# Kernel tuning notes

Hardware: AMD Instinct MI355X
Metric: run time of the kernel (lower is better)

Reference implementation:

```python
import jax, jax.numpy as jnp
import numpy as np

B, N, C, H = 8, 1024, 768, 12
HD = C // H  # 64


def setup_inputs() -> dict:
    key = jax.random.key(0)
    k0, k1, k2, k3, k4 = jax.random.split(key, 5)
    x = jax.random.normal(k0, (B, N, C), jnp.float32)
    # ToMe token sizes are counts >= 1; sample in [1, 16)
    size = jax.random.uniform(k1, (B, N, 1), jnp.float32, minval=1.0, maxval=16.0)
    key_padding_mask = jax.random.randint(k2, (B, N), 0, 2).astype(jnp.bool_)
    w_qkv = jax.random.normal(k3, (3 * C, C), jnp.float32) * (C ** -0.5)
    w_proj = jax.random.normal(k4, (C, C), jnp.float32) * (C ** -0.5)
    b_proj = jnp.zeros((C,), jnp.float32)
    return dict(x=x, size=size, key_padding_mask=key_padding_mask,
                w_qkv=w_qkv, w_proj=w_proj, b_proj=b_proj)


def reference(x, size, key_padding_mask, w_qkv, w_proj, b_proj):
    b, n, c = x.shape
    hd = c // H
    scale = hd ** -0.5
    # qkv projection: [B,N,3C] -> [3,B,H,N,hd]
    qkv = (x @ w_qkv.T).reshape(b, n, 3, H, hd).transpose(2, 0, 3, 1, 4)
    q, k, v = qkv[0], qkv[1], qkv[2]
    # raw scores [B,H,N,N]
    attn = jnp.einsum('bhnd,bhmd->bhnm', q, k) * scale
    # proportional attention: additive log-size bias over keys
    attn = attn + jnp.log(size)[:, None, None, :, 0]
    # key padding mask: True -> -inf
    attn = jnp.where(key_padding_mask[:, None, None, :], -jnp.inf, attn)
    attn = jax.nn.softmax(attn, axis=-1)
    # PV, back to [B,N,C]
    out = jnp.einsum('bhnm,bhmd->bnhd', attn, v).reshape(b, n, c)
    out = out @ w_proj.T + b_proj
    # mean of k over heads: [B,N,hd]
    k_mean = k.mean(axis=1)
    return out, k_mean
```

## Files before the change

### kernel.cpp

```cpp
#include <hip/hip_runtime.h>

typedef __bf16 bf16;
typedef __bf16 bf16x4 __attribute__((ext_vector_type(4)));
typedef __bf16 bf16x8 __attribute__((ext_vector_type(8)));
typedef float f32x4 __attribute__((ext_vector_type(4)));

#define MFMA_16x16x32(a, b, c) __builtin_amdgcn_mfma_f32_16x16x32_bf16((a), (b), (c), 0, 0, 0)

#define B_ 8
#define N_ 1024
#define C_ 768
#define H_ 12
#define HD_ 64
#define KDIM 768

__device__ __forceinline__ void gload_lds16(const void* g, void* l) {
  __builtin_amdgcn_global_load_lds(
      (const __attribute__((address_space(1))) void*)g,
      (__attribute__((address_space(3))) void*)l, 16, 0, 0);
}

__global__ __launch_bounds__(256) void detect_mask_kernel(const unsigned* __restrict__ m32,
                                                          int* __restrict__ flags) {
  const int i = blockIdx.x * 256 + threadIdx.x;
  if (i < 2048) {
    const unsigned v = m32[i];
    if (v > 1u) atomicOr(&flags[0], 1);
    if ((i & 1) && v != 0u) atomicOr(&flags[1], 1);
  }
}

__global__ __launch_bounds__(256) void cvt_kernel(const float* __restrict__ x,
                                                  const float* __restrict__ wq,
                                                  const float* __restrict__ wp,
                                                  const float* __restrict__ size_in,
                                                  const void* __restrict__ mask_raw,
                                                  const int* __restrict__ flags,
                                                  bf16* __restrict__ xb,
                                                  bf16* __restrict__ wqb,
                                                  bf16* __restrict__ wpb,
                                                  float* __restrict__ biasb) {
  const int i = blockIdx.x * 256 + threadIdx.x;
  {
    const float4 v = ((const float4*)x)[i];
    bf16x4 o = {(bf16)v.x, (bf16)v.y, (bf16)v.z, (bf16)v.w};
    ((bf16x4*)xb)[i] = o;
  }
  if (i < 442368) {
    const float4 v = ((const float4*)wq)[i];
    bf16x4 o = {(bf16)v.x, (bf16)v.y, (bf16)v.z, (bf16)v.w};
    ((bf16x4*)wqb)[i] = o;
  }
  if (i < 147456) {
    const float4 v = ((const float4*)wp)[i];
    bf16x4 o = {(bf16)v.x, (bf16)v.y, (bf16)v.z, (bf16)v.w};
    ((bf16x4*)wpb)[i] = o;
  }
  if (i < B_ * N_) {
    int mv;
    if (flags[0]) {
      mv = (int)((const unsigned char*)mask_raw)[i];
    } else if (flags[1]) {
      mv = ((const int*)mask_raw)[i];
    } else {
      const unsigned* m32 = (const unsigned*)mask_raw;
      mv = (int)(m32[2 * i] | m32[2 * i + 1]);
    }
    biasb[i] = mv ? -1e30f : logf(size_in[i]);
  }
}

template <int MODE>
__global__ __launch_bounds__(256) void gemm_bt(const bf16* __restrict__ A,
                                               const bf16* __restrict__ W,
                                               const float* __restrict__ bias,
                                               bf16* __restrict__ out0,
                                               bf16* __restrict__ out1,
                                               bf16* __restrict__ out2,
                                               float* __restrict__ outf) {
  __shared__ bf16 As[128 * 64];
  __shared__ bf16 Bs[128 * 64];
  const int bid = blockIdx.x;
  const int mt = bid % 64;
  const int nt = bid / 64;
  const int t = threadIdx.x;
  const int lane = t & 63, w = t >> 6;
  const int wm = w >> 1, wn = w & 1;
  const int l15 = lane & 15, lg = lane >> 4;

  f32x4 acc[4][4] = {};

  const int srow = t >> 3;
  const int skel = (t & 7) * 8;
  const bf16* Ag = A + (size_t)(mt * 128) * KDIM;
  const bf16* Bg = W + (size_t)(nt * 128) * KDIM;
  const int bA = mt >> 3;
  const int nbase = (mt & 7) * 128;

  for (int kt = 0; kt < KDIM; kt += 64) {
#pragma unroll
    for (int c = 0; c < 4; ++c) {
      const bf16* aSrc;
      if (MODE == 0)
        aSrc = Ag + (size_t)(c * 32 + srow) * KDIM + kt + skel;
      else
        aSrc = A + (((size_t)(bA * 12 + (kt >> 6)) * 1024) + nbase + c * 32 + srow) * 64 + skel;
      gload_lds16(aSrc, (char*)As + c * 4096 + w * 1024);
      gload_lds16(Bg + (size_t)(c * 32 + srow) * KDIM + kt + skel,
                  (char*)Bs + c * 4096 + w * 1024);
    }
    __syncthreads();
#pragma unroll
    for (int ks = 0; ks < 2; ++ks) {
      bf16x8 af[4], bfr[4];
#pragma unroll
      for (int i = 0; i < 4; ++i)
        af[i] = *(const bf16x8*)(As + (wm * 64 + i * 16 + l15) * 64 + ks * 32 + lg * 8);
#pragma unroll
      for (int i = 0; i < 4; ++i)
        bfr[i] = *(const bf16x8*)(Bs + (wn * 64 + i * 16 + l15) * 64 + ks * 32 + lg * 8);
#pragma unroll
      for (int i = 0; i < 4; ++i)
#pragma unroll
        for (int j = 0; j < 4; ++j)
          acc[i][j] = MFMA_16x16x32(af[i], bfr[j], acc[i][j]);
    }
    __syncthreads();
  }

  if (MODE == 0) {
    const int which = (nt * 128) / 768;
#pragma unroll
    for (int i = 0; i < 4; ++i)
#pragma unroll
      for (int j = 0; j < 4; ++j)
#pragma unroll
        for (int r = 0; r < 4; ++r) {
          const int m = mt * 128 + wm * 64 + i * 16 + lg * 4 + r;
          const int o = nt * 128 + wn * 64 + j * 16 + l15;
          const int b = m >> 10, n = m & 1023;
          const int f = o - which * 768;
          const int h = f >> 6, hd = f & 63;
          const bf16 bv = (bf16)acc[i][j][r];
          if (which == 0)
            out0[(((size_t)(b * 12 + h)) * 1024 + n) * 64 + hd] = bv;
          else if (which == 1)
            out1[(((size_t)(b * 12 + h)) * 1024 + n) * 64 + hd] = bv;
          else
            out2[(((size_t)(b * 12 + h)) * 64 + hd) * 1024 + n] = bv;
        }
  } else {
#pragma unroll
    for (int i = 0; i < 4; ++i)
#pragma unroll
      for (int j = 0; j < 4; ++j) {
        const int o = nt * 128 + wn * 64 + j * 16 + l15;
        const float bv = bias[o];
#pragma unroll
        for (int r = 0; r < 4; ++r) {
          const int m = mt * 128 + wm * 64 + i * 16 + lg * 4 + r;
          outf[(size_t)m * 768 + o] = acc[i][j][r] + bv;
        }
      }
  }
}

__global__ __launch_bounds__(256) void kmean_kernel(const bf16* __restrict__ kbuf,
                                                    float* __restrict__ kmean) {
  const int i = blockIdx.x * 256 + threadIdx.x;
  if (i >= B_ * N_ * HD_) return;
  const int hd = i & 63;
  const int n = (i >> 6) & 1023;
  const int b = i >> 16;
  float s = 0.f;
#pragma unroll
  for (int h = 0; h < 12; ++h)
    s += (float)kbuf[(((size_t)(b * 12 + h)) * 1024 + n) * 64 + hd];
  kmean[i] = s * (1.0f / 12.0f);
}

__global__ __launch_bounds__(512, 4) void attn_mfma(const bf16* __restrict__ qbuf,
                                                    const bf16* __restrict__ kbuf,
                                                    const bf16* __restrict__ vtbuf,
                                                    const float* __restrict__ biasb,
                                                    bf16* __restrict__ outws) {
  __shared__ bf16 Ks[2][4096];
  __shared__ bf16 Vs[2][4096];
  const int id = blockIdx.x;
  const int qt = id & 3;
  const int bh = id >> 2;
  const int b = bh / 12;
  const int t = threadIdx.x, lane = t & 63, w = t >> 6;
  const int l15 = lane & 15, lg = lane >> 4;
  const int qbase = qt * 256 + w * 16;

  const bf16* Q = qbuf + ((size_t)bh * 1024 + qbase) * 64;
  const bf16* Kp = kbuf + (size_t)bh * 65536;
  const bf16* Vt = vtbuf + (size_t)bh * 65536;
  const float* bias = biasb + b * 1024;

  const bf16x8 qb0 = *(const bf16x8*)(Q + l15 * 64 + lg * 8);
  const bf16x8 qb1 = *(const bf16x8*)(Q + l15 * 64 + 32 + lg * 8);
  const bf16x8 qc0 = *(const bf16x8*)(Q + (128 + l15) * 64 + lg * 8);
  const bf16x8 qc1 = *(const bf16x8*)(Q + (128 + l15) * 64 + 32 + lg * 8);

  const int srow = t >> 3;
  const int dsl = (t & 7) ^ (srow & 7);
  const int kkey = 32 * ((srow >> 5) & 1) + 4 * ((srow >> 4) & 1) +
                   8 * ((srow >> 2) & 3) + (srow & 3);
  const bf16* srcK = Kp + kkey * 64 + dsl * 8;
  const bf16* srcV = Vt + (size_t)srow * 1024 + dsl * 8;

  gload_lds16(srcK, (char*)&Ks[0][0] + w * 1024);
  gload_lds16(srcV, (char*)&Vs[0][0] + w * 1024);
  __syncthreads();

  const int bb0 = 8 * lg;
  const int swz = l15 & 7;

  f32x4 oacc[4] = {}, oacc2[4] = {};
  float m = -1e30f, l = 0.f;
  float m2 = -1e30f, l2 = 0.f;

  for (int kt = 0; kt < 16; ++kt) {
    const int cur = kt & 1;
    const int kb = kt * 64;
    if (kt < 15) {
      gload_lds16(srcK + (size_t)(kb + 64) * 64, (char*)&Ks[cur ^ 1][0] + w * 1024);
      gload_lds16(srcV + (kb + 64), (char*)&Vs[cur ^ 1][0] + w * 1024);
    }

    const bf16* LK = Ks[cur];
    const bf16* LV = Vs[cur];
    float sv[4][4], sw[4][4];
#pragma unroll
    for (int f = 0; f < 4; ++f) {
      const int cf = 32 * (f >> 1) + 4 * (f & 1);
      const bf16* kj = LK + (f * 16 + l15) * 64;
      const bf16x8 ka0 = *(const bf16x8*)(kj + (lg ^ swz) * 8);
      const bf16x8 ka1 = *(const bf16x8*)(kj + ((lg + 4) ^ swz) * 8);
      f32x4 z = {}, y = {};
      z = MFMA_16x16x32(ka0, qb0, z);
      y = MFMA_16x16x32(ka0, qc0, y);
      z = MFMA_16x16x32(ka1, qb1, z);
      y = MFMA_16x16x32(ka1, qc1, y);
      const float4 bi = *(const float4*)(bias + kb + cf + bb0);
      sv[f][0] = z[0] * 0.125f + bi.x;
      sv[f][1] = z[1] * 0.125f + bi.y;
      sv[f][2] = z[2] * 0.125f + bi.z;
      sv[f][3] = z[3] * 0.125f + bi.w;
      sw[f][0] = y[0] * 0.125f + bi.x;
      sw[f][1] = y[1] * 0.125f + bi.y;
      sw[f][2] = y[2] * 0.125f + bi.z;
      sw[f][3] = y[3] * 0.125f + bi.w;
    }
    float mx = sv[0][0], mx2 = sw[0][0];
#pragma unroll
    for (int f = 0; f < 4; ++f)
#pragma unroll
      for (int j = 0; j < 4; ++j) {
        mx = fmaxf(mx, sv[f][j]);
        mx2 = fmaxf(mx2, sw[f][j]);
      }
    mx = fmaxf(mx, __shfl_xor(mx, 16, 64));
    mx = fmaxf(mx, __shfl_xor(mx, 32, 64));
    mx2 = fmaxf(mx2, __shfl_xor(mx2, 16, 64));
    mx2 = fmaxf(mx2, __shfl_xor(mx2, 32, 64));
    const float mn = fmaxf(m, mx);
    const float mn2 = fmaxf(m2, mx2);
    const float resc = __expf(m - mn);
    const float resc2 = __expf(m2 - mn2);
    m = mn;
    m2 = mn2;

    float rs = 0.f, rs2 = 0.f;
    bf16x8 pa0, pa1, pa2, pa3;
#pragma unroll
    for (int f = 0; f < 4; ++f)
#pragma unroll
      for (int j = 0; j < 4; ++j) {
        const float p = __expf(sv[f][j] - mn);
        const float p2 = __expf(sw[f][j] - mn2);
        rs += p;
        rs2 += p2;
        const bf16 pb = (bf16)p;
        const bf16 pb2 = (bf16)p2;
        if (f == 0) { pa0[j] = pb; pa2[j] = pb2; }
        else if (f == 1) { pa0[4 + j] = pb; pa2[4 + j] = pb2; }
        else if (f == 2) { pa1[j] = pb; pa3[j] = pb2; }
        else { pa1[4 + j] = pb; pa3[4 + j] = pb2; }
      }
    rs += __shfl_xor(rs, 16, 64);
    rs += __shfl_xor(rs, 32, 64);
    rs2 += __shfl_xor(rs2, 16, 64);
    rs2 += __shfl_xor(rs2, 32, 64);
    l = l * resc + rs;
    l2 = l2 * resc2 + rs2;

#pragma unroll
    for (int df = 0; df < 4; ++df) {
      const bf16* vj = LV + (df * 16 + l15) * 64;
      const bf16x8 va0 = *(const bf16x8*)(vj + (lg ^ swz) * 8);
      const bf16x8 va1 = *(const bf16x8*)(vj + ((lg + 4) ^ swz) * 8);
      f32x4 t4 = oacc[df];
      f32x4 u4 = oacc2[df];
#pragma unroll
      for (int j = 0; j < 4; ++j) {
        t4[j] *= resc;
        u4[j] *= resc2;
      }
      t4 = MFMA_16x16x32(va0, pa0, t4);
      u4 = MFMA_16x16x32(va0, pa2, u4);
      t4 = MFMA_16x16x32(va1, pa1, t4);
      u4 = MFMA_16x16x32(va1, pa3, u4);
      oacc[df] = t4;
      oacc2[df] = u4;
    }
    __syncthreads();
  }

  const float inv = 1.0f / l;
  const float inv2 = 1.0f / l2;
  bf16* outp = outws + ((size_t)bh * 1024 + qbase + l15) * 64;
#pragma unroll
  for (int df = 0; df < 4; ++df) {
    bf16x4 ov = {(bf16)(oacc[df][0] * inv), (bf16)(oacc[df][1] * inv),
                 (bf16)(oacc[df][2] * inv), (bf16)(oacc[df][3] * inv)};
    *(bf16x4*)(outp + df * 16 + lg * 4) = ov;
    bf16x4 ov2 = {(bf16)(oacc2[df][0] * inv2), (bf16)(oacc2[df][1] * inv2),
                  (bf16)(oacc2[df][2] * inv2), (bf16)(oacc2[df][3] * inv2)};
    *(bf16x4*)(outp + (size_t)128 * 64 + df * 16 + lg * 4) = ov2;
  }
}

extern "C" void kernel_launch(void* const* d_in, const int* in_sizes, int n_in,
                              void* d_out, int out_size, void* d_ws, size_t ws_size,
                              hipStream_t stream) {
  const float* x       = (const float*)d_in[0];
  const float* size_in = (const float*)d_in[1];
  const void*  mask    = d_in[2];
  const float* w_qkv   = (const float*)d_in[3];
  const float* w_proj  = (const float*)d_in[4];
  const float* b_proj  = (const float*)d_in[5];
  float* out = (float*)d_out;

  if (n_in < 6 ||
      in_sizes[0] != 6291456 || in_sizes[1] != 8192 || in_sizes[2] != 8192 ||
      in_sizes[3] != 1769472 || in_sizes[4] != 589824 || in_sizes[5] != 768)
    return;

  const size_t QS = (size_t)B_ * H_ * N_ * HD_;
  if (ws_size < 55083024) return;

  bf16* xb    = (bf16*)d_ws;
  bf16* qbuf  = xb + QS;
  bf16* kbuf  = qbuf + QS;
  bf16* vtbuf = kbuf + QS;
  bf16* wqb   = vtbuf + QS;
  bf16* wpb   = wqb + 1769472;
  float* biasb = (float*)(wpb + 589824);
  int* flags = (int*)(biasb + 8192);
  bf16* attnw = xb;

  hipMemsetAsync(flags, 0, 8, stream);
  detect_mask_kernel<<<8, 256, 0, stream>>>((const unsigned*)mask, flags);
  cvt_kernel<<<6144, 256, 0, stream>>>(x, w_qkv, w_proj, size_in, mask, flags,
                                       xb, wqb, wpb, biasb);
  gemm_bt<0><<<64 * 18, 256, 0, stream>>>(xb, wqb, nullptr, qbuf, kbuf, vtbuf, nullptr);
  kmean_kernel<<<2048, 256, 0, stream>>>(kbuf, out + (size_t)B_ * N_ * C_);
  attn_mfma<<<384, 512, 0, stream>>>(qbuf, kbuf, vtbuf, biasb, attnw);
  gemm_bt<1><<<64 * 6, 256, 0, stream>>>(attnw, wpb, b_proj, nullptr, nullptr, nullptr, out);
}
```

Baseline: 176.9 us.

## Double-buffer LDS tiles in projection GEMM to overlap loads with MFMA

The GEMM now keeps two LDS stages for the A and B tiles. It issues the global-to-LDS loads for the next k-step before computing on the current stage, so each iteration needs one barrier instead of two. The goal is to hide global memory latency behind the MFMA work. In exchange, LDS use doubles to 64KB per block, which may lower occupancy.

```diff
diff --git a/kernel.cpp b/kernel.cpp
--- a/kernel.cpp
+++ b/kernel.cpp
@@ -78,8 +78,8 @@
                                                bf16* __restrict__ out1,
                                                bf16* __restrict__ out2,
                                                float* __restrict__ outf) {
-  __shared__ bf16 As[128 * 64];
-  __shared__ bf16 Bs[128 * 64];
+  __shared__ bf16 As[2][128 * 64];
+  __shared__ bf16 Bs[2][128 * 64];
   const int bid = blockIdx.x;
   const int mt = bid % 64;
   const int nt = bid / 64;
@@ -97,28 +97,38 @@
   const int bA = mt >> 3;
   const int nbase = (mt & 7) * 128;
 
-  for (int kt = 0; kt < KDIM; kt += 64) {
-#pragma unroll
-    for (int c = 0; c < 4; ++c) {
-      const bf16* aSrc;
-      if (MODE == 0)
-        aSrc = Ag + (size_t)(c * 32 + srow) * KDIM + kt + skel;
-      else
-        aSrc = A + (((size_t)(bA * 12 + (kt >> 6)) * 1024) + nbase + c * 32 + srow) * 64 + skel;
-      gload_lds16(aSrc, (char*)As + c * 4096 + w * 1024);
-      gload_lds16(Bg + (size_t)(c * 32 + srow) * KDIM + kt + skel,
-                  (char*)Bs + c * 4096 + w * 1024);
-    }
-    __syncthreads();
+#define ASRC(st, c)                                                          \
+  ((MODE == 0)                                                               \
+       ? (Ag + (size_t)((c) * 32 + srow) * KDIM + (st) * 64 + skel)          \
+       : (A + (((size_t)(bA * 12 + (st)) * 1024) + nbase + (c) * 32 + srow)  \
+              * 64 + skel))
+#define BSRC(st, c) (Bg + (size_t)((c) * 32 + srow) * KDIM + (st) * 64 + skel)
+
+#pragma unroll
+  for (int c = 0; c < 4; ++c) {
+    gload_lds16(ASRC(0, c), (char*)As[0] + c * 4096 + w * 1024);
+    gload_lds16(BSRC(0, c), (char*)Bs[0] + c * 4096 + w * 1024);
+  }
+  __syncthreads();
+
+  for (int st = 0; st < KDIM / 64; ++st) {
+    const int cur = st & 1;
+    if (st < KDIM / 64 - 1) {
+#pragma unroll
+      for (int c = 0; c < 4; ++c) {
+        gload_lds16(ASRC(st + 1, c), (char*)As[cur ^ 1] + c * 4096 + w * 1024);
+        gload_lds16(BSRC(st + 1, c), (char*)Bs[cur ^ 1] + c * 4096 + w * 1024);
+      }
+    }
 #pragma unroll
     for (int ks = 0; ks < 2; ++ks) {
       bf16x8 af[4], bfr[4];
 #pragma unroll
       for (int i = 0; i < 4; ++i)
-        af[i] = *(const bf16x8*)(As + (wm * 64 + i * 16 + l15) * 64 + ks * 32 + lg * 8);
+        af[i] = *(const bf16x8*)(As[cur] + (wm * 64 + i * 16 + l15) * 64 + ks * 32 + lg * 8);
 #pragma unroll
       for (int i = 0; i < 4; ++i)
-        bfr[i] = *(const bf16x8*)(Bs + (wn * 64 + i * 16 + l15) * 64 + ks * 32 + lg * 8);
+        bfr[i] = *(const bf16x8*)(Bs[cur] + (wn * 64 + i * 16 + l15) * 64 + ks * 32 + lg * 8);
 #pragma unroll
       for (int i = 0; i < 4; ++i)
 #pragma unroll
@@ -127,6 +137,8 @@
     }
     __syncthreads();
   }
+#undef ASRC
+#undef BSRC
 
   if (MODE == 0) {
     const int which = (nt * 128) / 768;
```

New measurement: 170.7 us. -3.5%, faster.
